# Performance work log

Hardware: AMD Instinct MI355X
Metric: run time of the kernel (lower is better)

Reference implementation:

```python
import jax, jax.numpy as jnp
import numpy as np


def setup_inputs() -> dict:
    key = jax.random.key(0)
    kx, kw = jax.random.split(key)
    x = jax.random.normal(kx, (32, 2048, 256), dtype=jnp.float32)
    W = jax.random.normal(kw, (1024, 256), dtype=jnp.float32)  # codebook [K, D]
    return {"x": x, "W": W}


def reference(x, W):
    D = W.shape[1]
    flat = x.reshape(-1, D)  # [N, D]
    # Squared Euclidean distances [N, K]; argmin is identical to cdist argmin.
    d2 = (
        jnp.sum(flat * flat, axis=1, keepdims=True)
        - 2.0 * (flat @ W.T)
        + jnp.sum(W * W, axis=1)
    )
    idx = jnp.argmin(d2, axis=1)  # [N]
    quant = W[idx].reshape(x.shape)  # direct gather == one-hot @ W
    # Straight-through estimator
    quantized = x + jax.lax.stop_gradient(quant - x)
    e_latent = jnp.mean((jax.lax.stop_gradient(quantized) - x) ** 2)
    q_latent = jnp.mean((quantized - jax.lax.stop_gradient(x)) ** 2)
    commitment_cost = 0.25
    loss = q_latent + commitment_cost * e_latent
    return quantized, loss, idx[:, None]
```

## Files before the change

### kernel.cpp

```cpp
#include <hip/hip_runtime.h>


#define NROWS    65536
#define DDIM     256
#define KCODES   1024
#define DEXT     512
#define ND_TOTAL 16777216

typedef __attribute__((ext_vector_type(8))) short bf16x8;
typedef __attribute__((ext_vector_type(4))) float floatx4;

__device__ __forceinline__ unsigned short f2bf(float f) {
    unsigned int u = __float_as_uint(f);
    return (unsigned short)((u + 0x7FFFu + ((u >> 16) & 1u)) >> 16);
}
__device__ __forceinline__ float bf2f(unsigned short h) {
    return __uint_as_float((unsigned int)h << 16);
}
__device__ __forceinline__ void split4(float4 v, ushort4* hi, ushort4* lo) {
    unsigned short hx = f2bf(v.x), hy = f2bf(v.y), hz = f2bf(v.z), hw = f2bf(v.w);
    *hi = make_ushort4(hx, hy, hz, hw);
    *lo = make_ushort4(f2bf(v.x - bf2f(hx)), f2bf(v.y - bf2f(hy)),
                       f2bf(v.z - bf2f(hz)), f2bf(v.w - bf2f(hw)));
}
__device__ __forceinline__ void async_copy16(void* lds, const void* g) {
    __builtin_amdgcn_global_load_lds(
        (const __attribute__((address_space(1))) unsigned int*)g,
        (__attribute__((address_space(3))) unsigned int*)lds, 16, 0, 0);
}

__device__ __forceinline__ void merge2(float& v1, int& k1, float& v2, int& k2,
                                       float o1, int ok1, float o2, int ok2) {
    bool aw = (v1 < o1) || (v1 == o1 && k1 < ok1);
    float ca = aw ? v2 : v1; int kca = aw ? k2 : k1;
    float cb = aw ? o1 : o2; int kcb = aw ? ok1 : ok2;
    float nv1 = aw ? v1 : o1; int nk1 = aw ? k1 : ok1;
    bool cw = (ca < cb) || (ca == cb && kca < kcb);
    v1 = nv1; k1 = nk1;
    v2 = cw ? ca : cb; k2 = cw ? kca : kcb;
}

__global__ void vq_prepw(const float* __restrict__ W, unsigned short* __restrict__ What,
                         float* __restrict__ w2, float* __restrict__ w2m,
                         float* __restrict__ lossws) {
    int k = blockIdx.x * 256 + threadIdx.x;
    if (k == 0) lossws[0] = 0.0f;
    if (k >= KCODES) return;
    const float4* wr = (const float4*)(W + (size_t)k * DDIM);
    unsigned short* hrow = What + (size_t)k * DEXT;
    float s = 0.0f;
    for (int i = 0; i < 64; ++i) {
        float4 v = wr[i];
        s = fmaf(v.x, v.x, s); s = fmaf(v.y, v.y, s);
        s = fmaf(v.z, v.z, s); s = fmaf(v.w, v.w, s);
        ushort4 hv, lv;
        split4(v, &hv, &lv);
        *(ushort4*)(hrow + i * 4) = hv;
        *(ushort4*)(hrow + 256 + i * 4) = lv;
    }
    w2[k] = s;
    w2m[k] = s - 256.0f;
}

__global__ void vq_convx(const float* __restrict__ x, unsigned short* Xhat) {
    int gid = blockIdx.x * 256 + threadIdx.x;
    int row = gid >> 6, q = gid & 63;
    float4 v = ((const float4*)x)[gid];
    ushort4 hv, lv;
    split4(v, &hv, &lv);
    unsigned short* r = Xhat + (size_t)row * DEXT;
    *(ushort4*)(r + q * 4) = hv;
    *(ushort4*)(r + 256 + q * 4) = lv;
}

__global__ __launch_bounds__(256, 2) void vq_main(
    const unsigned short* Xhat, const unsigned short* __restrict__ What,
    const float* __restrict__ x, const float* __restrict__ W,
    const float* __restrict__ w2, const float* __restrict__ w2m,
    float* qout, float* lossws, float* idx_out)
{
    __shared__ unsigned short As[128 * 32];
    __shared__ unsigned short Bs[128 * 32];
    __shared__ float Wm[KCODES];
    __shared__ float rv1[2][128], rv2[2][128];
    __shared__ int   rk1[2][128], rk2[2][128];
    __shared__ int   candk[128][4];
    __shared__ float resc[128][4];
    __shared__ int   fink[128];

    const int tid  = threadIdx.x;
    const int wave = tid >> 6, lane = tid & 63;
    const int quad = lane >> 4, l15 = lane & 15;
    const int wr = wave >> 1, wc = wave & 1;
    const int row0 = blockIdx.x * 128;

    #pragma unroll
    for (int t = 0; t < 4; ++t) Wm[t * 256 + tid] = w2m[t * 256 + tid];

    float s1[16], s2[16];
    #pragma unroll
    for (int s = 0; s < 16; ++s) { s1[s] = 3.0e38f; s2[s] = 3.0e38f; }

    const int g0 = wave * 64 + lane, g1 = 256 + g0;
    const int r0 = g0 >> 2, p0 = g0 & 3;
    const int r1 = g1 >> 2, p1 = g1 & 3;
    const unsigned short* Ab = Xhat + (size_t)row0 * DEXT;

    #pragma unroll 1
    for (int ct = 0; ct < 8; ++ct) {
        floatx4 acc[4][4];
        #pragma unroll
        for (int i = 0; i < 4; ++i)
            #pragma unroll
            for (int j = 0; j < 4; ++j) acc[i][j] = (floatx4){0.f, 0.f, 0.f, 0.f};

        const unsigned short* Bb = What + (size_t)(ct * 128) * DEXT;

        #pragma unroll 1
        for (int p = 0; p < 2; ++p) {
            const int bswap = p << 8;
            #pragma unroll 1
            for (int dc = 0; dc < DEXT; dc += 32) {
                const int bdc = dc ^ bswap;
                __syncthreads();
                async_copy16(As + g0 * 8, Ab + (size_t)r0 * DEXT + dc + p0 * 8);
                async_copy16(As + g1 * 8, Ab + (size_t)r1 * DEXT + dc + p1 * 8);
                async_copy16(Bs + g0 * 8, Bb + (size_t)r0 * DEXT + bdc + p0 * 8);
                async_copy16(Bs + g1 * 8, Bb + (size_t)r1 * DEXT + bdc + p1 * 8);
                __syncthreads();
                bf16x8 a[4], b[4];
                #pragma unroll
                for (int i = 0; i < 4; ++i)
                    a[i] = *(const bf16x8*)(As + ((wr * 64 + i * 16 + l15) * 32 + quad * 8));
                #pragma unroll
                for (int j = 0; j < 4; ++j)
                    b[j] = *(const bf16x8*)(Bs + ((wc * 64 + j * 16 + l15) * 32 + quad * 8));
                #pragma unroll
                for (int i = 0; i < 4; ++i)
                    #pragma unroll
                    for (int j = 0; j < 4; ++j)
                        acc[i][j] = __builtin_amdgcn_mfma_f32_16x16x32_bf16(a[i], b[j], acc[i][j], 0, 0, 0);
            }
        }

        #pragma unroll
        for (int j = 0; j < 4; ++j) {
            int c = ct * 128 + wc * 64 + j * 16 + l15;
            float wm = Wm[c];
            unsigned pay = (unsigned)((j << 3) | ct);
            #pragma unroll
            for (int i = 0; i < 4; ++i)
                #pragma unroll
                for (int r = 0; r < 4; ++r) {
                    float v = fmaf(-2.0f, acc[i][j][r], wm);
                    float pf = __uint_as_float((__float_as_uint(v) & 0xFFFFFFE0u) | pay);
                    int s = i * 4 + r;
                    float t = fminf(s1[s], pf);
                    s2[s] = fminf(s2[s], fmaxf(s1[s], pf));
                    s1[s] = t;
                }
        }
    }

    float v1[16], v2[16];
    int k1[16], k2[16];
    #pragma unroll
    for (int s = 0; s < 16; ++s) {
        unsigned u1 = __float_as_uint(s1[s]) & 31u;
        unsigned u2 = __float_as_uint(s2[s]) & 31u;
        v1[s] = s1[s]; v2[s] = s2[s];
        k1[s] = (int)(u1 & 7u) * 128 + wc * 64 + (int)(u1 >> 3) * 16 + l15;
        k2[s] = (int)(u2 & 7u) * 128 + wc * 64 + (int)(u2 >> 3) * 16 + l15;
    }
    #pragma unroll
    for (int m = 1; m < 16; m <<= 1) {
        #pragma unroll
        for (int s = 0; s < 16; ++s) {
            float o1 = __shfl_xor(v1[s], m, 64);
            int  ok1 = __shfl_xor(k1[s], m, 64);
            float o2 = __shfl_xor(v2[s], m, 64);
            int  ok2 = __shfl_xor(k2[s], m, 64);
            merge2(v1[s], k1[s], v2[s], k2[s], o1, ok1, o2, ok2);
        }
    }
    if (l15 == 0) {
        #pragma unroll
        for (int s = 0; s < 16; ++s) {
            int row = wr * 64 + (s >> 2) * 16 + quad * 4 + (s & 3);
            rv1[wc][row] = v1[s]; rk1[wc][row] = k1[s];
            rv2[wc][row] = v2[s]; rk2[wc][row] = k2[s];
        }
    }
    __syncthreads();
    if (tid < 128) {
        candk[tid][0] = rk1[0][tid];
        candk[tid][1] = rk2[0][tid];
        candk[tid][2] = rk1[1][tid];
        candk[tid][3] = rk2[1][tid];
    }
    __syncthreads();
    #pragma unroll
    for (int j2 = 0; j2 < 2; ++j2) {
        int job = tid + j2 * 256;
        int r = job >> 2, cn = job & 3;
        int k = candk[r][cn];
        const float4* xr  = (const float4*)(x + (size_t)(row0 + r) * DDIM);
        const float4* wrp = (const float4*)(W + (size_t)k * DDIM);
        float dot = 0.0f;
        #pragma unroll 8
        for (int i = 0; i < 64; ++i) {
            float4 va = xr[i], vb = wrp[i];
            dot = fmaf(va.x, vb.x, dot); dot = fmaf(va.y, vb.y, dot);
            dot = fmaf(va.z, vb.z, dot); dot = fmaf(va.w, vb.w, dot);
        }
        resc[r][cn] = fmaf(-2.0f, dot, w2[k]);
    }
    __syncthreads();
    if (tid < 128) {
        float bd = resc[tid][0];
        int   bk = candk[tid][0];
        #pragma unroll
        for (int cn = 1; cn < 4; ++cn) {
            float d = resc[tid][cn];
            int   k = candk[tid][cn];
            if (d < bd || (d == bd && k < bk)) { bd = d; bk = k; }
        }
        fink[tid] = bk;
        idx_out[row0 + tid] = (float)bk;
    }
    __syncthreads();

    const int c4 = tid & 63, rsub = tid >> 6;
    float lsum = 0.0f;
    for (int it2 = 0; it2 < 32; ++it2) {
        int r = it2 * 4 + rsub;
        int k = fink[r];
        float4 wv = ((const float4*)(W + (size_t)k * DDIM))[c4];
        float4 xv = ((const float4*)(x + (size_t)(row0 + r) * DDIM))[c4];
        ((float4*)(qout + (size_t)(row0 + r) * DDIM))[c4] = wv;
        float dx = wv.x - xv.x, dy = wv.y - xv.y;
        float dz = wv.z - xv.z, dw = wv.w - xv.w;
        lsum = fmaf(dx, dx, lsum); lsum = fmaf(dy, dy, lsum);
        lsum = fmaf(dz, dz, lsum); lsum = fmaf(dw, dw, lsum);
    }
    #pragma unroll
    for (int off = 32; off > 0; off >>= 1) lsum += __shfl_down(lsum, off, 64);
    if (lane == 0) atomicAdd(lossws, lsum);
}

__global__ void vq_fin(const float* __restrict__ lossws, float* __restrict__ loss_out) {
    loss_out[0] = 1.25f * lossws[0] / (float)ND_TOTAL;
}

extern "C" void kernel_launch(void* const* d_in, const int* in_sizes, int n_in,
                              void* d_out, int out_size, void* d_ws, size_t ws_size,
                              hipStream_t stream) {
    const float* x = (const float*)d_in[0];
    const float* W = (const float*)d_in[1];
    float* out = (float*)d_out;
    unsigned short* Xhat = (unsigned short*)d_out;
    unsigned short* What = (unsigned short*)d_ws;
    float* w2     = (float*)((char*)d_ws + (1 << 20));
    float* w2m    = w2 + 1024;
    float* lossws = w2 + 2048;
    float* idx_out = out + (size_t)ND_TOTAL + 1;

    vq_prepw<<<4, 256, 0, stream>>>(W, What, w2, w2m, lossws);
    vq_convx<<<16384, 256, 0, stream>>>(x, Xhat);
    vq_main<<<512, 256, 0, stream>>>(Xhat, What, x, W, w2, w2m, out, lossws, idx_out);
    vq_fin<<<1, 1, 0, stream>>>(lossws, out + ND_TOTAL);
}
```

Before: 398.3 us.

## Double-buffer GEMM tiles with async prefetch, LDS swizzle, and fused hi/lo MFMAs

```diff
diff --git a/kernel.cpp b/kernel.cpp
--- a/kernel.cpp
+++ b/kernel.cpp
@@ -79,14 +79,16 @@
     const float* __restrict__ w2, const float* __restrict__ w2m,
     float* qout, float* lossws, float* idx_out)
 {
-    __shared__ unsigned short As[128 * 32];
-    __shared__ unsigned short Bs[128 * 32];
+    __shared__ __align__(16) unsigned short smem[2 * 4 * 128 * 32];
     __shared__ float Wm[KCODES];
-    __shared__ float rv1[2][128], rv2[2][128];
-    __shared__ int   rk1[2][128], rk2[2][128];
-    __shared__ int   candk[128][4];
-    __shared__ float resc[128][4];
-    __shared__ int   fink[128];
+
+    float* rv1   = (float*)smem;
+    float* rv2   = rv1 + 256;
+    int*   rk1   = (int*)(rv2 + 256);
+    int*   rk2   = rk1 + 256;
+    int*   candk = rk2 + 256;
+    float* resc  = (float*)(candk + 512);
+    int*   fink  = (int*)(resc + 512);
 
     const int tid  = threadIdx.x;
     const int wave = tid >> 6, lane = tid & 63;
@@ -101,64 +103,96 @@
     #pragma unroll
     for (int s = 0; s < 16; ++s) { s1[s] = 3.0e38f; s2[s] = 3.0e38f; }
 
-    const int g0 = wave * 64 + lane, g1 = 256 + g0;
-    const int r0 = g0 >> 2, p0 = g0 & 3;
-    const int r1 = g1 >> 2, p1 = g1 & 3;
+    const int r0 = tid >> 2, p0 = tid & 3;
+    const int psw = (p0 ^ ((r0 >> 1) & 3)) << 3;
+    const int quadS8 = (quad ^ ((l15 >> 1) & 3)) << 3;
     const unsigned short* Ab = Xhat + (size_t)row0 * DEXT;
 
+    auto STAGE = [&](int q, int cb) {
+        const int ct = q >> 3, dc = (q & 7) << 5;
+        const unsigned short* An = Ab + (size_t)r0 * DEXT + dc + psw;
+        const unsigned short* Bn = What + ((size_t)(ct * 128 + r0)) * DEXT + dc + psw;
+        unsigned short* L = smem + cb * 16384 + tid * 8;
+        async_copy16(L,          An);
+        async_copy16(L + 2048,   An + 64 * DEXT);
+        async_copy16(L + 4096,   An + 256);
+        async_copy16(L + 6144,   An + 64 * DEXT + 256);
+        async_copy16(L + 8192,   Bn);
+        async_copy16(L + 10240,  Bn + 64 * DEXT);
+        async_copy16(L + 12288,  Bn + 256);
+        async_copy16(L + 14336,  Bn + 64 * DEXT + 256);
+    };
+
+    STAGE(0, 0);
+    STAGE(1, 1);
+
+    floatx4 acc[4][4];
+    #pragma unroll
+    for (int i = 0; i < 4; ++i)
+        #pragma unroll
+        for (int j = 0; j < 4; ++j) acc[i][j] = (floatx4){0.f, 0.f, 0.f, 0.f};
+
     #pragma unroll 1
-    for (int ct = 0; ct < 8; ++ct) {
-        floatx4 acc[4][4];
+    for (int q = 0; q < 64; ++q) {
+        const int cb = q & 1;
+        if (q != 63) { asm volatile("s_waitcnt vmcnt(8)" ::: "memory"); }
+        else         { asm volatile("s_waitcnt vmcnt(0)" ::: "memory"); }
+        __builtin_amdgcn_s_barrier();
+        asm volatile("" ::: "memory");
+        __builtin_amdgcn_s_setprio(1);
+
+        const unsigned short* Sb = smem + cb * 16384;
+        bf16x8 a0[4], a1[4], b0[4], b1[4];
+        #pragma unroll
+        for (int i = 0; i < 4; ++i) {
+            const int ro = (wr * 64 + i * 16 + l15) * 32 + quadS8;
+            a0[i] = *(const bf16x8*)(Sb + ro);
+            a1[i] = *(const bf16x8*)(Sb + 4096 + ro);
+        }
+        #pragma unroll
+        for (int j = 0; j < 4; ++j) {
+            const int ro = (wc * 64 + j * 16 + l15) * 32 + quadS8;
+            b0[j] = *(const bf16x8*)(Sb + 8192 + ro);
+            b1[j] = *(const bf16x8*)(Sb + 12288 + ro);
+        }
         #pragma unroll
         for (int i = 0; i < 4; ++i)
             #pragma unroll
-            for (int j = 0; j < 4; ++j) acc[i][j] = (floatx4){0.f, 0.f, 0.f, 0.f};
-
-        const unsigned short* Bb = What + (size_t)(ct * 128) * DEXT;
-
-        #pragma unroll 1
-        for (int p = 0; p < 2; ++p) {
-            const int bswap = p << 8;
-            #pragma unroll 1
-            for (int dc = 0; dc < DEXT; dc += 32) {
-                const int bdc = dc ^ bswap;
-                __syncthreads();
-                async_copy16(As + g0 * 8, Ab + (size_t)r0 * DEXT + dc + p0 * 8);
-                async_copy16(As + g1 * 8, Ab + (size_t)r1 * DEXT + dc + p1 * 8);
-                async_copy16(Bs + g0 * 8, Bb + (size_t)r0 * DEXT + bdc + p0 * 8);
-                async_copy16(Bs + g1 * 8, Bb + (size_t)r1 * DEXT + bdc + p1 * 8);
-                __syncthreads();
-                bf16x8 a[4], b[4];
-                #pragma unroll
-                for (int i = 0; i < 4; ++i)
-                    a[i] = *(const bf16x8*)(As + ((wr * 64 + i * 16 + l15) * 32 + quad * 8));
-                #pragma unroll
-                for (int j = 0; j < 4; ++j)
-                    b[j] = *(const bf16x8*)(Bs + ((wc * 64 + j * 16 + l15) * 32 + quad * 8));
+            for (int j = 0; j < 4; ++j) {
+                acc[i][j] = __builtin_amdgcn_mfma_f32_16x16x32_bf16(a0[i], b0[j], acc[i][j], 0, 0, 0);
+                acc[i][j] = __builtin_amdgcn_mfma_f32_16x16x32_bf16(a1[i], b1[j], acc[i][j], 0, 0, 0);
+                acc[i][j] = __builtin_amdgcn_mfma_f32_16x16x32_bf16(a0[i], b1[j], acc[i][j], 0, 0, 0);
+                acc[i][j] = __builtin_amdgcn_mfma_f32_16x16x32_bf16(a1[i], b0[j], acc[i][j], 0, 0, 0);
+            }
+        __builtin_amdgcn_s_setprio(0);
+        asm volatile("s_waitcnt lgkmcnt(0)" ::: "memory");
+        __builtin_amdgcn_s_barrier();
+        asm volatile("" ::: "memory");
+        if (q + 2 < 64) STAGE(q + 2, cb);
+
+        if ((q & 7) == 7) {
+            const int ctf = q >> 3;
+            #pragma unroll
+            for (int j = 0; j < 4; ++j) {
+                int cc = ctf * 128 + wc * 64 + j * 16 + l15;
+                float wm = Wm[cc];
+                unsigned pay = (unsigned)((j << 3) | ctf);
                 #pragma unroll
                 for (int i = 0; i < 4; ++i)
                     #pragma unroll
-                    for (int j = 0; j < 4; ++j)
-                        acc[i][j] = __builtin_amdgcn_mfma_f32_16x16x32_bf16(a[i], b[j], acc[i][j], 0, 0, 0);
+                    for (int r = 0; r < 4; ++r) {
+                        float v = fmaf(-2.0f, acc[i][j][r], wm);
+                        float pf = __uint_as_float((__float_as_uint(v) & 0xFFFFFFE0u) | pay);
+                        int s = i * 4 + r;
+                        float t = fminf(s1[s], pf);
+                        s2[s] = fminf(s2[s], fmaxf(s1[s], pf));
+                        s1[s] = t;
+                    }
             }
-        }
-
-        #pragma unroll
-        for (int j = 0; j < 4; ++j) {
-            int c = ct * 128 + wc * 64 + j * 16 + l15;
-            float wm = Wm[c];
-            unsigned pay = (unsigned)((j << 3) | ct);
             #pragma unroll
             for (int i = 0; i < 4; ++i)
                 #pragma unroll
-                for (int r = 0; r < 4; ++r) {
-                    float v = fmaf(-2.0f, acc[i][j][r], wm);
-                    float pf = __uint_as_float((__float_as_uint(v) & 0xFFFFFFE0u) | pay);
-                    int s = i * 4 + r;
-                    float t = fminf(s1[s], pf);
-                    s2[s] = fminf(s2[s], fmaxf(s1[s], pf));
-                    s1[s] = t;
-                }
+                for (int j = 0; j < 4; ++j) acc[i][j] = (floatx4){0.f, 0.f, 0.f, 0.f};
         }
     }
 
@@ -187,23 +221,23 @@
         #pragma unroll
         for (int s = 0; s < 16; ++s) {
             int row = wr * 64 + (s >> 2) * 16 + quad * 4 + (s & 3);
-            rv1[wc][row] = v1[s]; rk1[wc][row] = k1[s];
-            rv2[wc][row] = v2[s]; rk2[wc][row] = k2[s];
+            rv1[wc * 128 + row] = v1[s]; rk1[wc * 128 + row] = k1[s];
+            rv2[wc * 128 + row] = v2[s]; rk2[wc * 128 + row] = k2[s];
         }
     }
     __syncthreads();
     if (tid < 128) {
-        candk[tid][0] = rk1[0][tid];
-        candk[tid][1] = rk2[0][tid];
-        candk[tid][2] = rk1[1][tid];
-        candk[tid][3] = rk2[1][tid];
+        candk[tid * 4 + 0] = rk1[tid];
+        candk[tid * 4 + 1] = rk2[tid];
+        candk[tid * 4 + 2] = rk1[128 + tid];
+        candk[tid * 4 + 3] = rk2[128 + tid];
     }
     __syncthreads();
     #pragma unroll
     for (int j2 = 0; j2 < 2; ++j2) {
         int job = tid + j2 * 256;
         int r = job >> 2, cn = job & 3;
-        int k = candk[r][cn];
+        int k = candk[r * 4 + cn];
         const float4* xr  = (const float4*)(x + (size_t)(row0 + r) * DDIM);
         const float4* wrp = (const float4*)(W + (size_t)k * DDIM);
         float dot = 0.0f;
@@ -213,16 +247,16 @@
             dot = fmaf(va.x, vb.x, dot); dot = fmaf(va.y, vb.y, dot);
             dot = fmaf(va.z, vb.z, dot); dot = fmaf(va.w, vb.w, dot);
         }
-        resc[r][cn] = fmaf(-2.0f, dot, w2[k]);
+        resc[r * 4 + cn] = fmaf(-2.0f, dot, w2[k]);
     }
     __syncthreads();
     if (tid < 128) {
-        float bd = resc[tid][0];
-        int   bk = candk[tid][0];
+        float bd = resc[tid * 4 + 0];
+        int   bk = candk[tid * 4 + 0];
         #pragma unroll
         for (int cn = 1; cn < 4; ++cn) {
-            float d = resc[tid][cn];
-            int   k = candk[tid][cn];
+            float d = resc[tid * 4 + cn];
+            int   k = candk[tid * 4 + cn];
             if (d < bd || (d == bd && k < bk)) { bd = d; bk = k; }
         }
         fink[tid] = bk;
```

Result: faster. 336.2 us (-15.6%).
